# Optimization experiments

Measured on AMD Instinct MI355X. Metric: run time of the kernel, lower is better.

## Reference

```python
import jax, jax.numpy as jnp
import numpy as np

EMBED_DIM = 768
NUM_HEADS = 12
HEAD_DIM = EMBED_DIM // NUM_HEADS


def setup_inputs() -> dict:
    key = jax.random.key(0)
    ks = jax.random.split(key, 9)
    B, S, D = 2, 2048, EMBED_DIM
    scale = 1.0 / np.sqrt(D)
    x = jax.random.normal(ks[0], (B, S, D), dtype=jnp.float32)
    Wq = jax.random.normal(ks[1], (D, D), dtype=jnp.float32) * scale
    bq = jax.random.normal(ks[2], (D,), dtype=jnp.float32) * 0.01
    Wk = jax.random.normal(ks[3], (D, D), dtype=jnp.float32) * scale
    bk = jax.random.normal(ks[4], (D,), dtype=jnp.float32) * 0.01
    Wv = jax.random.normal(ks[5], (D, D), dtype=jnp.float32) * scale
    bv = jax.random.normal(ks[6], (D,), dtype=jnp.float32) * 0.01
    Wo = jax.random.normal(ks[7], (D, D), dtype=jnp.float32) * scale
    bo = jax.random.normal(ks[8], (D,), dtype=jnp.float32) * 0.01
    return {"x": x, "Wq": Wq, "bq": bq, "Wk": Wk, "bk": bk,
            "Wv": Wv, "bv": bv, "Wo": Wo, "bo": bo}


def reference(x, Wq, bq, Wk, bk, Wv, bv, Wo, bo):
    B, S, D = x.shape
    H, Dh = NUM_HEADS, HEAD_DIM
    # separate QKV projections (weights stored [in, out] so y = x @ W + b)
    q = (x @ Wq + bq).reshape(B, S, H, Dh)
    k = (x @ Wk + bk).reshape(B, S, H, Dh)
    v = (x @ Wv + bv).reshape(B, S, H, Dh)
    # NOTE: original module applies NO 1/sqrt(head_dim) scaling
    scores = jnp.einsum('bqhd,bkhd->bhqk', q, k)          # [B,H,S,S] materialized
    attn = jax.nn.softmax(scores, axis=-1)
    ctx = jnp.einsum('bhqk,bkhd->bqhd', attn, v)          # [B,S,H,Dh]
    out = ctx.reshape(B, S, D) @ Wo + bo
    return out
```

## Files before the change

kernel.cpp:

```cpp
#include <hip/hip_runtime.h>
#include <hip/hip_bf16.h>


typedef __attribute__((ext_vector_type(8))) short short8;
typedef __attribute__((ext_vector_type(4))) float float4e;

__device__ __forceinline__ ushort f2bf(float f) {
    union { float f; unsigned u; } v; v.f = f;
    unsigned r = v.u + 0x7FFF + ((v.u >> 16) & 1);
    return (ushort)(r >> 16);
}

__device__ __forceinline__ unsigned pk2bf(float a, float b) {
    float2 t; t.x = a; t.y = b;
    __hip_bfloat162 h = __float22bfloat162_rn(t);
    union { __hip_bfloat162 h; unsigned u; } cv; cv.h = h;
    return cv.u;
}

__device__ __forceinline__ void async_cp16(const ushort* g, ushort* l) {
    __builtin_amdgcn_global_load_lds(
        (const __attribute__((address_space(1))) unsigned int*)g,
        (__attribute__((address_space(3))) unsigned int*)l,
        16, 0, 0);
}

__global__ __launch_bounds__(256) void cast_f32_bf16(
    const float* __restrict__ in, ushort* __restrict__ out, int n4)
{
    int i = blockIdx.x * blockDim.x + threadIdx.x;
    if (i < n4) {
        float4 v = *(const float4*)&in[(size_t)i * 4];
        ushort4 o;
        o.x = f2bf(v.x); o.y = f2bf(v.y); o.z = f2bf(v.z); o.w = f2bf(v.w);
        *(ushort4*)&out[(size_t)i * 4] = o;
    }
}

__global__ __launch_bounds__(256) void transpose_cast_w4(
    const float* __restrict__ W0, const float* __restrict__ W1,
    const float* __restrict__ W2, const float* __restrict__ W3,
    ushort* __restrict__ WtBase)
{
    __shared__ float t[64][65];
    const int z = blockIdx.z;
    const float* W = (z == 0) ? W0 : (z == 1) ? W1 : (z == 2) ? W2 : W3;
    ushort* Wt = WtBase + (size_t)z * (768u * 768u);

    const int tid = threadIdx.x;
    const int c  = tid & 63;
    const int rg = tid >> 6;
    const int k0 = blockIdx.y * 64, n0 = blockIdx.x * 64;
    #pragma unroll
    for (int r = 0; r < 16; ++r) {
        const int row = rg * 16 + r;
        t[row][c] = W[(size_t)(k0 + row) * 768 + n0 + c];
    }
    __syncthreads();
    #pragma unroll
    for (int r = 0; r < 16; ++r) {
        const int row = rg * 16 + r;
        Wt[(size_t)(n0 + row) * 768 + k0 + c] = f2bf(t[c][row]);
    }
}

__global__ __launch_bounds__(256) void transpose_v(
    const ushort* __restrict__ Vb, ushort* __restrict__ VT)
{
    __shared__ ushort t[64][72];
    const int tid = threadIdx.x;
    const int b = blockIdx.z, h = blockIdx.y, s0 = blockIdx.x * 64;
    const int lr = tid >> 3;
    const int lc = (tid & 7) * 8;

    #pragma unroll
    for (int half = 0; half < 64; half += 32) {
        const int row = lr + half;
        *(uint4*)&t[row][lc] =
            *(const uint4*)&Vb[(size_t)(b * 2048 + s0 + row) * 768 + h * 64 + lc];
    }
    __syncthreads();
    #pragma unroll
    for (int half = 0; half < 64; half += 32) {
        const int d = lr + half;
        ushort tmp[8];
        #pragma unroll
        for (int i = 0; i < 8; ++i) tmp[i] = t[lc + i][d];
        *(uint4*)&VT[((size_t)(b * 12 + h) * 64 + d) * 2048 + s0 + lc] =
            *(const uint4*)tmp;
    }
}

__global__ __launch_bounds__(256) void gemm_qkv_fused(
    const ushort* __restrict__ A, const ushort* __restrict__ Bt,
    const float* __restrict__ bq, const float* __restrict__ bk,
    const float* __restrict__ bv, ushort* __restrict__ Outbase)
{
    constexpr int K = 768;
    __shared__ ushort As[128][32];
    __shared__ ushort Bs[128][32];

    const int tid  = threadIdx.x;
    const int w    = tid >> 6;
    const int lane = tid & 63;
    const int l16  = lane & 15;
    const int quad = lane >> 4;
    const int wr   = (w >> 1) * 64;
    const int wc   = (w & 1) * 64;
    const int row0 = blockIdx.y * 128, col0 = blockIdx.x * 128;

    const int r4 = lane >> 2;
    const int c8 = (lane & 3) * 8;

    float4e acc[4][4];
    #pragma unroll
    for (int mi = 0; mi < 4; ++mi)
        #pragma unroll
        for (int ni = 0; ni < 4; ++ni) acc[mi][ni] = (float4e){0.f,0.f,0.f,0.f};

    for (int k0 = 0; k0 < K; k0 += 32) {
        #pragma unroll
        for (int i = 0; i < 2; ++i) {
            const int rr = w * 32 + i * 16;
            async_cp16(&A [(size_t)(row0 + rr + r4) * K + k0 + c8], &As[rr][0]);
            async_cp16(&Bt[(size_t)(col0 + rr + r4) * K + k0 + c8], &Bs[rr][0]);
        }
        __syncthreads();

        short8 af[4], bf[4];
        #pragma unroll
        for (int i = 0; i < 4; ++i) {
            af[i] = *(const short8*)&As[wr + i * 16 + l16][quad * 8];
            bf[i] = *(const short8*)&Bs[wc + i * 16 + l16][quad * 8];
        }
        #pragma unroll
        for (int mi = 0; mi < 4; ++mi)
            #pragma unroll
            for (int ni = 0; ni < 4; ++ni)
                acc[mi][ni] = __builtin_amdgcn_mfma_f32_16x16x32_bf16(
                    af[mi], bf[ni], acc[mi][ni], 0, 0, 0);
        __syncthreads();
    }

    const int seg = (col0 >= 1536) ? 2 : (col0 >= 768 ? 1 : 0);
    const float* bias = (seg == 0) ? bq : (seg == 1) ? bk : bv;
    const int ncol0 = col0 - seg * 768 + wc;
    ushort* outp = Outbase + (size_t)seg * (4096u * 768u);

    #pragma unroll
    for (int ni = 0; ni < 4; ++ni) {
        const int col = ncol0 + ni * 16 + l16;
        const float bs = bias[col];
        #pragma unroll
        for (int mi = 0; mi < 4; ++mi) {
            #pragma unroll
            for (int r = 0; r < 4; ++r) {
                const int row = row0 + wr + mi * 16 + quad * 4 + r;
                outp[(size_t)row * 768 + col] = f2bf(acc[mi][ni][r] + bs);
            }
        }
    }
}

__global__ __launch_bounds__(256) void gemm_wo_128(
    const ushort* __restrict__ A, const ushort* __restrict__ Bt,
    const float* __restrict__ bias, float* __restrict__ Cout)
{
    constexpr int K = 768, N = 768;
    __shared__ ushort As[128][40];
    __shared__ ushort Bs[128][40];

    const int tid  = threadIdx.x;
    const int w    = tid >> 6;
    const int lane = tid & 63;
    const int l16  = lane & 15;
    const int quad = lane >> 4;
    const int wr   = (w >> 1) * 64;
    const int wc   = (w & 1) * 64;
    const int row0 = blockIdx.y * 128, col0 = blockIdx.x * 128;
    const int sr = tid >> 2, sc = (tid & 3) * 8;

    float4e acc[4][4];
    #pragma unroll
    for (int mi = 0; mi < 4; ++mi)
        #pragma unroll
        for (int ni = 0; ni < 4; ++ni) acc[mi][ni] = (float4e){0.f,0.f,0.f,0.f};

    uint4 a0 = *(const uint4*)&A [(size_t)(row0 + sr     ) * K + sc];
    uint4 a1 = *(const uint4*)&A [(size_t)(row0 + sr + 64) * K + sc];
    uint4 b0 = *(const uint4*)&Bt[(size_t)(col0 + sr     ) * K + sc];
    uint4 b1 = *(const uint4*)&Bt[(size_t)(col0 + sr + 64) * K + sc];

    for (int k0 = 0; k0 < K; k0 += 32) {
        *(uint4*)&As[sr     ][sc] = a0;
        *(uint4*)&As[sr + 64][sc] = a1;
        *(uint4*)&Bs[sr     ][sc] = b0;
        *(uint4*)&Bs[sr + 64][sc] = b1;
        __syncthreads();

        if (k0 + 32 < K) {
            const int kn = k0 + 32;
            a0 = *(const uint4*)&A [(size_t)(row0 + sr     ) * K + kn + sc];
            a1 = *(const uint4*)&A [(size_t)(row0 + sr + 64) * K + kn + sc];
            b0 = *(const uint4*)&Bt[(size_t)(col0 + sr     ) * K + kn + sc];
            b1 = *(const uint4*)&Bt[(size_t)(col0 + sr + 64) * K + kn + sc];
        }

        short8 af[4], bf[4];
        #pragma unroll
        for (int i = 0; i < 4; ++i) {
            af[i] = *(const short8*)&As[wr + i * 16 + l16][quad * 8];
            bf[i] = *(const short8*)&Bs[wc + i * 16 + l16][quad * 8];
        }
        #pragma unroll
        for (int mi = 0; mi < 4; ++mi)
            #pragma unroll
            for (int ni = 0; ni < 4; ++ni)
                acc[mi][ni] = __builtin_amdgcn_mfma_f32_16x16x32_bf16(
                    af[mi], bf[ni], acc[mi][ni], 0, 0, 0);
        __syncthreads();
    }

    #pragma unroll
    for (int ni = 0; ni < 4; ++ni) {
        const int col = col0 + wc + ni * 16 + l16;
        const float bs = bias[col];
        #pragma unroll
        for (int mi = 0; mi < 4; ++mi) {
            #pragma unroll
            for (int r = 0; r < 4; ++r) {
                const int row = row0 + wr + mi * 16 + quad * 4 + r;
                Cout[(size_t)row * N + col] = acc[mi][ni][r] + bs;
            }
        }
    }
}

__global__ __launch_bounds__(512) void attn_mfma(
    const ushort* __restrict__ Qg, const ushort* __restrict__ Kgl,
    const ushort* __restrict__ VT, ushort* __restrict__ Ctx)
{
    constexpr int S = 2048, D = 768;
    __shared__ union {
        struct {
            ushort Ks [2][64][64];
            ushort Vts[2][64][64];
        } s;
        struct {
            float Osc[4][16][68];
            float Msc[4][16], Lsc[4][16];
        } c;
    } U;
    __shared__ ushort Ps[64][64];

    const int tid  = threadIdx.x;
    const int w    = tid >> 6;
    const int wq   = w & 3;
    const int koff = (w >> 2) * 32;
    const int lane = tid & 63;
    const int l16  = lane & 15;
    const int quad = lane >> 4;
    const int b = blockIdx.z, h = blockIdx.y, q0 = blockIdx.x * 64;
    const size_t hc = (size_t)h * 64;

    const size_t qoff = (size_t)(b * S + q0 + wq * 16 + l16) * D + hc + quad * 8;
    const short8 yq0 = *(const short8*)&Qg[qoff];
    const short8 yq1 = *(const short8*)&Qg[qoff + 32];

    const int sr  = tid >> 3;
    const int cbg = (tid & 7) ^ (sr & 7);
    const ushort* srcK = &Kgl[(size_t)(b * S + sr) * D + hc + cbg * 8];
    const ushort* srcV = &VT[((size_t)(b * 12 + h) * 64 + sr) * 2048 + cbg * 8];
    ushort* dstK0 = &U.s.Ks [0][w * 8][0];
    ushort* dstK1 = &U.s.Ks [1][w * 8][0];
    ushort* dstV0 = &U.s.Vts[0][w * 8][0];
    ushort* dstV1 = &U.s.Vts[1][w * 8][0];

    int oxk[2][2];
    #pragma unroll
    for (int kb = 0; kb < 2; ++kb) {
        const int krow = koff + kb * 16 + l16;
        oxk[kb][0] = krow * 64 + (( quad     ) ^ (krow & 7)) * 8;
        oxk[kb][1] = krow * 64 + (((quad | 4)) ^ (krow & 7)) * 8;
    }
    const int oxv0 = l16 * 64 + ((((koff >> 3) + quad)) ^ (l16 & 7)) * 8;
    const int prow = wq * 16 + l16;
    const int pxor = (prow & 7) * 2;
    const int opw0 = prow * 64 + ((((koff >> 2)     + quad)) ^ pxor) * 4;
    const int opw1 = prow * 64 + ((((koff >> 2) + 4 + quad)) ^ pxor) * 4;
    const int opr  = prow * 64 + ((((koff >> 2) + quad * 2)) ^ pxor) * 4;

    float m_ = -1e30f, l_ = 0.f;
    float4e oa[4];
    #pragma unroll
    for (int n = 0; n < 4; ++n) oa[n] = (float4e){0.f, 0.f, 0.f, 0.f};

    async_cp16(srcK, dstK0);
    async_cp16(srcV, dstV0);
    __syncthreads();

    #pragma unroll 2
    for (int k0 = 0; k0 < S; k0 += 64) {
        const int cur = (k0 >> 6) & 1;
        if (k0 + 64 < S) {
            async_cp16(srcK + (size_t)(k0 + 64) * D, cur ? dstK0 : dstK1);
            async_cp16(srcV + (k0 + 64),             cur ? dstV0 : dstV1);
        }
        const ushort* ksb = cur ? &U.s.Ks [1][0][0] : &U.s.Ks [0][0][0];
        const ushort* vsb = cur ? &U.s.Vts[1][0][0] : &U.s.Vts[0][0][0];

        float4e sa[2];
        __builtin_amdgcn_s_setprio(1);
        #pragma unroll
        for (int kb = 0; kb < 2; ++kb) {
            const short8 xk0 = *(const short8*)&ksb[oxk[kb][0]];
            const short8 xk1 = *(const short8*)&ksb[oxk[kb][1]];
            float4e z = (float4e){0.f, 0.f, 0.f, 0.f};
            z      = __builtin_amdgcn_mfma_f32_16x16x32_bf16(xk0, yq0, z, 0, 0, 0);
            sa[kb] = __builtin_amdgcn_mfma_f32_16x16x32_bf16(xk1, yq1, z, 0, 0, 0);
        }
        __builtin_amdgcn_s_setprio(0);

        float mx = -1e30f;
        #pragma unroll
        for (int kb = 0; kb < 2; ++kb)
            #pragma unroll
            for (int r = 0; r < 4; ++r) mx = fmaxf(mx, sa[kb][r]);
        mx = fmaxf(mx, __shfl_xor(mx, 16, 64));
        mx = fmaxf(mx, __shfl_xor(mx, 32, 64));

        const bool full = !__all(mx - m_ <= 8.f);
        float alpha = 0.f;
        if (full) {
            const float mn = fmaxf(m_, mx);
            alpha = __expf(m_ - mn);
            l_ *= alpha;
            m_ = mn;
        }

        float p[2][4], ps = 0.f;
        #pragma unroll
        for (int kb = 0; kb < 2; ++kb)
            #pragma unroll
            for (int r = 0; r < 4; ++r) {
                p[kb][r] = __expf(sa[kb][r] - m_);
                ps += p[kb][r];
            }

        {
            uint2 pk;
            pk.x = pk2bf(p[0][0], p[0][1]);
            pk.y = pk2bf(p[0][2], p[0][3]);
            *(uint2*)&Ps[0][opw0] = pk;
            pk.x = pk2bf(p[1][0], p[1][1]);
            pk.y = pk2bf(p[1][2], p[1][3]);
            *(uint2*)&Ps[0][opw1] = pk;
        }

        ps += __shfl_xor(ps, 16, 64);
        ps += __shfl_xor(ps, 32, 64);
        l_ += ps;

        if (full) {
            #pragma unroll
            for (int n = 0; n < 4; ++n)
                #pragma unroll
                for (int r = 0; r < 4; ++r) oa[n][r] *= alpha;
        }

        const short8 yp = *(const short8*)&Ps[0][opr];
        __builtin_amdgcn_s_setprio(1);
        #pragma unroll
        for (int db = 0; db < 4; ++db) {
            const short8 xv = *(const short8*)&vsb[oxv0 + db * 1024];
            oa[db] = __builtin_amdgcn_mfma_f32_16x16x32_bf16(xv, yp, oa[db], 0, 0, 0);
        }
        __builtin_amdgcn_s_setprio(0);

        __syncthreads();
    }

    if (w >= 4) {
        if (quad == 0) { U.c.Msc[wq][l16] = m_; U.c.Lsc[wq][l16] = l_; }
        #pragma unroll
        for (int db = 0; db < 4; ++db)
            *(float4*)&U.c.Osc[wq][l16][db * 16 + quad * 4] =
                *(const float4*)&oa[db];
    }
    __syncthreads();
    if (w < 4) {
        const float m1 = U.c.Msc[wq][l16], l1 = U.c.Lsc[wq][l16];
        const float mm = fmaxf(m_, m1);
        const float a0 = __expf(m_ - mm), a1 = __expf(m1 - mm);
        const float inv = 1.0f / (l_ * a0 + l1 * a1);
        const size_t crow = (size_t)(b * S + q0 + wq * 16 + l16) * D + hc;
        #pragma unroll
        for (int db = 0; db < 4; ++db) {
            const float4 o1 = *(const float4*)&U.c.Osc[wq][l16][db * 16 + quad * 4];
            uint2 ov;
            ov.x = pk2bf((oa[db][0] * a0 + o1.x * a1) * inv,
                         (oa[db][1] * a0 + o1.y * a1) * inv);
            ov.y = pk2bf((oa[db][2] * a0 + o1.z * a1) * inv,
                         (oa[db][3] * a0 + o1.w * a1) * inv);
            *(uint2*)&Ctx[crow + db * 16 + quad * 4] = ov;
        }
    }
}

extern "C" void kernel_launch(void* const* d_in, const int* in_sizes, int n_in,
                              void* d_out, int out_size, void* d_ws, size_t ws_size,
                              hipStream_t stream)
{
    const float* x  = (const float*)d_in[0];
    const float* Wq = (const float*)d_in[1];
    const float* bq = (const float*)d_in[2];
    const float* Wk = (const float*)d_in[3];
    const float* bk = (const float*)d_in[4];
    const float* Wv = (const float*)d_in[5];
    const float* bv = (const float*)d_in[6];
    const float* Wo = (const float*)d_in[7];
    const float* bo = (const float*)d_in[8];

    const int M = 4096, D = 768;
    const size_t XE = (size_t)M * D;
    const size_t WE = (size_t)D * D;

    ushort* xb   = (ushort*)d_ws;
    ushort* wtq  = xb   + XE;
    ushort* wto  = wtq  + 3 * WE;
    ushort* qb   = wto  + WE;
    ushort* kb   = qb   + XE;
    ushort* vb   = kb   + XE;
    ushort* ctxb = vb   + XE;
    ushort* vt   = xb;

    cast_f32_bf16<<<(int)(XE / 4 / 256), 256, 0, stream>>>(x, xb, (int)(XE / 4));

    transpose_cast_w4<<<dim3(12, 12, 4), 256, 0, stream>>>(Wq, Wk, Wv, Wo, wtq);

    gemm_qkv_fused<<<dim3(2304 / 128, 4096 / 128), 256, 0, stream>>>(
        xb, wtq, bq, bk, bv, qb);

    transpose_v<<<dim3(32, 12, 2), 256, 0, stream>>>(vb, vt);

    attn_mfma<<<dim3(2048 / 64, 12, 2), 512, 0, stream>>>(qb, kb, vt, ctxb);

    gemm_wo_128<<<dim3(768 / 128, 4096 / 128), 256, 0, stream>>>(
        ctxb, wto, bo, (float*)d_out);
}
```

Before: 187.0 us.

## Fuse V transpose into QKV GEMM epilogue and process K in 64-wide steps

The QKV GEMM epilogue now writes the V segment straight into the transposed [b,h,d,s] layout using 4-element vector stores, so the separate transpose_v kernel launch and its extra read and write of V are gone. The GEMM main loop loads two 32-wide K slices per iteration into double LDS buffers, which halves the number of barrier pairs. The attention kernel moves the output rescale into the max-update branch. The transposed V stores are strided across rows, which may write less efficiently, and the added LDS use could lower occupancy.

New measurement: 187.9 us. No clear change (+0.5%).

```diff
diff --git a/kernel.cpp b/kernel.cpp
--- a/kernel.cpp
+++ b/kernel.cpp
@@ -64,41 +64,17 @@
     }
 }
 
-__global__ __launch_bounds__(256) void transpose_v(
-    const ushort* __restrict__ Vb, ushort* __restrict__ VT)
-{
-    __shared__ ushort t[64][72];
-    const int tid = threadIdx.x;
-    const int b = blockIdx.z, h = blockIdx.y, s0 = blockIdx.x * 64;
-    const int lr = tid >> 3;
-    const int lc = (tid & 7) * 8;
-
-    #pragma unroll
-    for (int half = 0; half < 64; half += 32) {
-        const int row = lr + half;
-        *(uint4*)&t[row][lc] =
-            *(const uint4*)&Vb[(size_t)(b * 2048 + s0 + row) * 768 + h * 64 + lc];
-    }
-    __syncthreads();
-    #pragma unroll
-    for (int half = 0; half < 64; half += 32) {
-        const int d = lr + half;
-        ushort tmp[8];
-        #pragma unroll
-        for (int i = 0; i < 8; ++i) tmp[i] = t[lc + i][d];
-        *(uint4*)&VT[((size_t)(b * 12 + h) * 64 + d) * 2048 + s0 + lc] =
-            *(const uint4*)tmp;
-    }
-}
-
 __global__ __launch_bounds__(256) void gemm_qkv_fused(
     const ushort* __restrict__ A, const ushort* __restrict__ Bt,
     const float* __restrict__ bq, const float* __restrict__ bk,
-    const float* __restrict__ bv, ushort* __restrict__ Outbase)
+    const float* __restrict__ bv, ushort* __restrict__ Outbase,
+    ushort* __restrict__ VTout)
 {
     constexpr int K = 768;
-    __shared__ ushort As[128][32];
-    __shared__ ushort Bs[128][32];
+    __shared__ ushort As0[128][32];
+    __shared__ ushort As1[128][32];
+    __shared__ ushort Bs0[128][32];
+    __shared__ ushort Bs1[128][32];
 
     const int tid  = threadIdx.x;
     const int w    = tid >> 6;
@@ -118,45 +94,85 @@
         #pragma unroll
         for (int ni = 0; ni < 4; ++ni) acc[mi][ni] = (float4e){0.f,0.f,0.f,0.f};
 
-    for (int k0 = 0; k0 < K; k0 += 32) {
+    for (int k0 = 0; k0 < K; k0 += 64) {
         #pragma unroll
         for (int i = 0; i < 2; ++i) {
             const int rr = w * 32 + i * 16;
-            async_cp16(&A [(size_t)(row0 + rr + r4) * K + k0 + c8], &As[rr][0]);
-            async_cp16(&Bt[(size_t)(col0 + rr + r4) * K + k0 + c8], &Bs[rr][0]);
+            const size_t ra = (size_t)(row0 + rr + r4) * K + k0 + c8;
+            const size_t rb = (size_t)(col0 + rr + r4) * K + k0 + c8;
+            async_cp16(&A [ra],      &As0[rr][0]);
+            async_cp16(&A [ra + 32], &As1[rr][0]);
+            async_cp16(&Bt[rb],      &Bs0[rr][0]);
+            async_cp16(&Bt[rb + 32], &Bs1[rr][0]);
         }
         __syncthreads();
 
-        short8 af[4], bf[4];
-        #pragma unroll
-        for (int i = 0; i < 4; ++i) {
-            af[i] = *(const short8*)&As[wr + i * 16 + l16][quad * 8];
-            bf[i] = *(const short8*)&Bs[wc + i * 16 + l16][quad * 8];
-        }
-        #pragma unroll
-        for (int mi = 0; mi < 4; ++mi)
-            #pragma unroll
-            for (int ni = 0; ni < 4; ++ni)
-                acc[mi][ni] = __builtin_amdgcn_mfma_f32_16x16x32_bf16(
-                    af[mi], bf[ni], acc[mi][ni], 0, 0, 0);
+        {
+            short8 af[4], bf[4];
+            #pragma unroll
+            for (int i = 0; i < 4; ++i) {
+                af[i] = *(const short8*)&As0[wr + i * 16 + l16][quad * 8];
+                bf[i] = *(const short8*)&Bs0[wc + i * 16 + l16][quad * 8];
+            }
+            #pragma unroll
+            for (int mi = 0; mi < 4; ++mi)
+                #pragma unroll
+                for (int ni = 0; ni < 4; ++ni)
+                    acc[mi][ni] = __builtin_amdgcn_mfma_f32_16x16x32_bf16(
+                        af[mi], bf[ni], acc[mi][ni], 0, 0, 0);
+        }
+        {
+            short8 af[4], bf[4];
+            #pragma unroll
+            for (int i = 0; i < 4; ++i) {
+                af[i] = *(const short8*)&As1[wr + i * 16 + l16][quad * 8];
+                bf[i] = *(const short8*)&Bs1[wc + i * 16 + l16][quad * 8];
+            }
+            #pragma unroll
+            for (int mi = 0; mi < 4; ++mi)
+                #pragma unroll
+                for (int ni = 0; ni < 4; ++ni)
+                    acc[mi][ni] = __builtin_amdgcn_mfma_f32_16x16x32_bf16(
+                        af[mi], bf[ni], acc[mi][ni], 0, 0, 0);
+        }
         __syncthreads();
     }
 
     const int seg = (col0 >= 1536) ? 2 : (col0 >= 768 ? 1 : 0);
     const float* bias = (seg == 0) ? bq : (seg == 1) ? bk : bv;
     const int ncol0 = col0 - seg * 768 + wc;
-    ushort* outp = Outbase + (size_t)seg * (4096u * 768u);
-
-    #pragma unroll
-    for (int ni = 0; ni < 4; ++ni) {
-        const int col = ncol0 + ni * 16 + l16;
-        const float bs = bias[col];
-        #pragma unroll
-        for (int mi = 0; mi < 4; ++mi) {
-            #pragma unroll
-            for (int r = 0; r < 4; ++r) {
-                const int row = row0 + wr + mi * 16 + quad * 4 + r;
-                outp[(size_t)row * 768 + col] = f2bf(acc[mi][ni][r] + bs);
+
+    if (seg < 2) {
+        ushort* outp = Outbase + (size_t)seg * (4096u * 768u);
+        #pragma unroll
+        for (int ni = 0; ni < 4; ++ni) {
+            const int col = ncol0 + ni * 16 + l16;
+            const float bs = bias[col];
+            #pragma unroll
+            for (int mi = 0; mi < 4; ++mi) {
+                #pragma unroll
+                for (int r = 0; r < 4; ++r) {
+                    const int row = row0 + wr + mi * 16 + quad * 4 + r;
+                    outp[(size_t)row * 768 + col] = f2bf(acc[mi][ni][r] + bs);
+                }
+            }
+        }
+    } else {
+        #pragma unroll
+        for (int ni = 0; ni < 4; ++ni) {
+            const int vcol = ncol0 + ni * 16 + l16;
+            const int hh = vcol >> 6, dd = vcol & 63;
+            const float bs = bias[vcol];
+            #pragma unroll
+            for (int mi = 0; mi < 4; ++mi) {
+                const int row = row0 + wr + mi * 16 + quad * 4;
+                const int bb = row >> 11, ss = row & 2047;
+                ushort4 o;
+                o.x = f2bf(acc[mi][ni][0] + bs);
+                o.y = f2bf(acc[mi][ni][1] + bs);
+                o.z = f2bf(acc[mi][ni][2] + bs);
+                o.w = f2bf(acc[mi][ni][3] + bs);
+                *(ushort4*)&VTout[((size_t)(bb * 12 + hh) * 64 + dd) * 2048 + ss] = o;
             }
         }
     }
@@ -330,12 +346,15 @@
         mx = fmaxf(mx, __shfl_xor(mx, 32, 64));
 
         const bool full = !__all(mx - m_ <= 8.f);
-        float alpha = 0.f;
         if (full) {
             const float mn = fmaxf(m_, mx);
-            alpha = __expf(m_ - mn);
+            const float alpha = __expf(m_ - mn);
             l_ *= alpha;
             m_ = mn;
+            #pragma unroll
+            for (int n = 0; n < 4; ++n)
+                #pragma unroll
+                for (int r = 0; r < 4; ++r) oa[n][r] *= alpha;
         }
 
         float p[2][4], ps = 0.f;
@@ -360,13 +379,6 @@
         ps += __shfl_xor(ps, 16, 64);
         ps += __shfl_xor(ps, 32, 64);
         l_ += ps;
-
-        if (full) {
-            #pragma unroll
-            for (int n = 0; n < 4; ++n)
-                #pragma unroll
-                for (int r = 0; r < 4; ++r) oa[n][r] *= alpha;
-        }
 
         const short8 yp = *(const short8*)&Ps[0][opr];
         __builtin_amdgcn_s_setprio(1);
@@ -430,18 +442,15 @@
     ushort* wto  = wtq  + 3 * WE;
     ushort* qb   = wto  + WE;
     ushort* kb   = qb   + XE;
-    ushort* vb   = kb   + XE;
-    ushort* ctxb = vb   + XE;
-    ushort* vt   = xb;
+    ushort* vt   = kb   + XE;
+    ushort* ctxb = vt   + XE;
 
     cast_f32_bf16<<<(int)(XE / 4 / 256), 256, 0, stream>>>(x, xb, (int)(XE / 4));
 
     transpose_cast_w4<<<dim3(12, 12, 4), 256, 0, stream>>>(Wq, Wk, Wv, Wo, wtq);
 
     gemm_qkv_fused<<<dim3(2304 / 128, 4096 / 128), 256, 0, stream>>>(
-        xb, wtq, bq, bk, bv, qb);
-
-    transpose_v<<<dim3(32, 12, 2), 256, 0, stream>>>(vb, vt);
+        xb, wtq, bq, bk, bv, qb, vt);
 
     attn_mfma<<<dim3(2048 / 64, 12, 2), 512, 0, stream>>>(qb, kb, vt, ctxb);
 
```

## Feed P directly from registers into PV MFMA, permuting V reads instead

Applied to the files above, without the earlier changes.

Removes the shared-memory round trip for the softmax probabilities P by packing them in registers and using them directly as the MFMA B operand. To make the register layout of P match the K-dimension ordering, the V^T tile is now read as two 8-byte chunks per lane with a matching permuted, swizzled index. The alpha rescale of the accumulators moves into the branch where alpha is computed. This trades one LDS write, one LDS read and the dependency through them for split 64-bit V loads, which may raise LDS instruction count or cause bank conflicts.

Result: slower. 191.7 us (+2.5%).

```diff
diff --git a/kernel.cpp b/kernel.cpp
--- a/kernel.cpp
+++ b/kernel.cpp
@@ -251,7 +251,6 @@
             float Msc[4][16], Lsc[4][16];
         } c;
     } U;
-    __shared__ ushort Ps[64][64];
 
     const int tid  = threadIdx.x;
     const int w    = tid >> 6;
@@ -283,12 +282,8 @@
         oxk[kb][0] = krow * 64 + (( quad     ) ^ (krow & 7)) * 8;
         oxk[kb][1] = krow * 64 + (((quad | 4)) ^ (krow & 7)) * 8;
     }
-    const int oxv0 = l16 * 64 + ((((koff >> 3) + quad)) ^ (l16 & 7)) * 8;
-    const int prow = wq * 16 + l16;
-    const int pxor = (prow & 7) * 2;
-    const int opw0 = prow * 64 + ((((koff >> 2)     + quad)) ^ pxor) * 4;
-    const int opw1 = prow * 64 + ((((koff >> 2) + 4 + quad)) ^ pxor) * 4;
-    const int opr  = prow * 64 + ((((koff >> 2) + quad * 2)) ^ pxor) * 4;
+    const int oxva = l16 * 64 + ((((koff >> 2)     + quad)) ^ ((l16 & 7) * 2)) * 4;
+    const int oxvb = l16 * 64 + ((((koff >> 2) + 4 + quad)) ^ ((l16 & 7) * 2)) * 4;
 
     float m_ = -1e30f, l_ = 0.f;
     float4e oa[4];
@@ -330,12 +325,15 @@
         mx = fmaxf(mx, __shfl_xor(mx, 32, 64));
 
         const bool full = !__all(mx - m_ <= 8.f);
-        float alpha = 0.f;
         if (full) {
             const float mn = fmaxf(m_, mx);
-            alpha = __expf(m_ - mn);
+            const float alpha = __expf(m_ - mn);
             l_ *= alpha;
             m_ = mn;
+            #pragma unroll
+            for (int n = 0; n < 4; ++n)
+                #pragma unroll
+                for (int r = 0; r < 4; ++r) oa[n][r] *= alpha;
         }
 
         float p[2][4], ps = 0.f;
@@ -347,33 +345,23 @@
                 ps += p[kb][r];
             }
 
-        {
-            uint2 pk;
-            pk.x = pk2bf(p[0][0], p[0][1]);
-            pk.y = pk2bf(p[0][2], p[0][3]);
-            *(uint2*)&Ps[0][opw0] = pk;
-            pk.x = pk2bf(p[1][0], p[1][1]);
-            pk.y = pk2bf(p[1][2], p[1][3]);
-            *(uint2*)&Ps[0][opw1] = pk;
-        }
+        union { unsigned u[4]; short8 s8; } pa;
+        pa.u[0] = pk2bf(p[0][0], p[0][1]);
+        pa.u[1] = pk2bf(p[0][2], p[0][3]);
+        pa.u[2] = pk2bf(p[1][0], p[1][1]);
+        pa.u[3] = pk2bf(p[1][2], p[1][3]);
 
         ps += __shfl_xor(ps, 16, 64);
         ps += __shfl_xor(ps, 32, 64);
         l_ += ps;
 
-        if (full) {
-            #pragma unroll
-            for (int n = 0; n < 4; ++n)
-                #pragma unroll
-                for (int r = 0; r < 4; ++r) oa[n][r] *= alpha;
-        }
-
-        const short8 yp = *(const short8*)&Ps[0][opr];
         __builtin_amdgcn_s_setprio(1);
         #pragma unroll
         for (int db = 0; db < 4; ++db) {
-            const short8 xv = *(const short8*)&vsb[oxv0 + db * 1024];
-            oa[db] = __builtin_amdgcn_mfma_f32_16x16x32_bf16(xv, yp, oa[db], 0, 0, 0);
+            union { uint2 v2[2]; short8 s8; } xv;
+            xv.v2[0] = *(const uint2*)&vsb[oxva + db * 1024];
+            xv.v2[1] = *(const uint2*)&vsb[oxvb + db * 1024];
+            oa[db] = __builtin_amdgcn_mfma_f32_16x16x32_bf16(xv.s8, pa.s8, oa[db], 0, 0, 0);
         }
         __builtin_amdgcn_s_setprio(0);
 
```
